# Optimization experiments

Hardware: AMD Instinct MI355X
Metric: run time of the kernel (lower is better)

Reference implementation:

```python
import jax, jax.numpy as jnp
import numpy as np

T, B, D = 1024, 64, 1024  # time steps, batch, num_inputs == num_hiddens
SIGMA = 0.01


def setup_inputs() -> dict:
    key = jax.random.key(0)
    ks = jax.random.split(key, 7)
    w = lambda k: (jax.random.normal(k, (D, D), dtype=jnp.float32) * SIGMA)
    return {
        "inputs": jax.random.normal(ks[0], (T, B, D), dtype=jnp.float32),
        "W_xz": w(ks[1]), "W_hz": w(ks[2]), "b_z": jnp.zeros((D,), jnp.float32),
        "W_xr": w(ks[3]), "W_hr": w(ks[4]), "b_r": jnp.zeros((D,), jnp.float32),
        "W_xh": w(ks[5]), "W_hh": w(ks[6]), "b_h": jnp.zeros((D,), jnp.float32),
    }


def reference(inputs, W_xz, W_hz, b_z, W_xr, W_hr, b_r, W_xh, W_hh, b_h):
    # Precompute all input-to-hidden projections in batched GEMMs (T*B rows).
    Xz = jnp.einsum('tbi,ih->tbh', inputs, W_xz) + b_z
    Xr = jnp.einsum('tbi,ih->tbh', inputs, W_xr) + b_r
    Xh = jnp.einsum('tbi,ih->tbh', inputs, W_xh) + b_h

    def step(H, xs):
        xz, xr, xh = xs
        Z = jax.nn.sigmoid(xz + H @ W_hz)
        R = jax.nn.sigmoid(xr + H @ W_hr)
        # torch precedence: R * H @ W_hh == R * (H @ W_hh)
        H_tilde = jnp.tanh(xh + R * (H @ W_hh))
        H_new = Z * H + (1.0 - Z) * H_tilde
        return H_new, H_new

    H0 = jnp.zeros((inputs.shape[1], inputs.shape[2]), dtype=inputs.dtype)
    H_last, outputs = jax.lax.scan(step, H0, (Xz, Xr, Xh))
    return outputs, H_last
```

## Files before the change

kernel.cpp:

```cpp
#include <hip/hip_runtime.h>
#include <hip/hip_bf16.h>
#include <stdint.h>

typedef unsigned int u32;
typedef unsigned short u16;
typedef short bf16x8 __attribute__((ext_vector_type(8)));
typedef float f32x4 __attribute__((ext_vector_type(4)));
typedef u32 u32x4 __attribute__((ext_vector_type(4)));

#define T_STEPS 1024
#define BATCH   64
#define DIM     1024
#define NGRP    8
#define GWG     32
#define NTHR    512

#define CTL_XCNT(x)   ((x)*16)
#define CTL_ARR       128
#define CTL_MODE      144
#define CTL_FLAG(g,w) (256 + ((g)*GWG + (w))*16)
#define CTL_U32       4608

__device__ __forceinline__ u16 f2bf(float f) {
  u32 u = __float_as_uint(f);
  return (u16)((u + 0x7FFFu + ((u >> 16) & 1u)) >> 16);
}
__device__ __forceinline__ float sigm(float x) { return 1.0f / (1.0f + __expf(-x)); }
__device__ __forceinline__ float tanh_f(float x) {
  x = fminf(8.0f, fmaxf(-8.0f, x));
  float e = __expf(2.0f * x);
  return (e - 1.0f) / (e + 1.0f);
}

__global__ void gru_init(u32* ctrl) {
  for (int i = threadIdx.x; i < CTL_U32; i += 512) ctrl[i] = 0;
}

__global__ void gru_xconv(const float* __restrict__ in, u32* __restrict__ xb) {
  size_t i = (size_t)(blockIdx.x * 256 + threadIdx.x) * 8;
  f32x4 lo = *(const f32x4*)(in + i);
  f32x4 hi = *(const f32x4*)(in + i + 4);
  u32x4 o;
  o[0] = ((u32)f2bf(lo[1]) << 16) | f2bf(lo[0]);
  o[1] = ((u32)f2bf(lo[3]) << 16) | f2bf(lo[2]);
  o[2] = ((u32)f2bf(hi[1]) << 16) | f2bf(hi[0]);
  o[3] = ((u32)f2bf(hi[3]) << 16) | f2bf(hi[2]);
  *(u32x4*)(xb + i / 2) = o;
}

__global__ void gru_pack3(const float* __restrict__ Wz, const float* __restrict__ Wr,
                          const float* __restrict__ Wh, u16* __restrict__ wp) {
  int idx = blockIdx.x * 256 + threadIdx.x;
  if (idx >= GWG * 8 * 2 * 3 * 4 * 64) return;
  int lane = idx & 63; int r = idx >> 6;
  int ks = r & 3; r >>= 2;
  int n = r % 3; r /= 3;
  int cg = r & 1; r >>= 1;
  int wv = r & 7; int wid = r >> 3;
  int k0 = wv * 128 + ks * 32 + (lane >> 4) * 8;
  int col = wid * 32 + cg * 16 + (lane & 15);
  const float* W = (n == 0) ? Wz : (n == 1) ? Wr : Wh;
  u16* dst = wp + (size_t)idx * 8;
#pragma unroll
  for (int j = 0; j < 8; ++j) dst[j] = f2bf(W[(size_t)(k0 + j) * DIM + col]);
}

#define WAIT0 asm volatile("s_waitcnt vmcnt(0)" ::: "memory"); __builtin_amdgcn_sched_barrier(0)
#define MFMA_(A, B, C) __builtin_amdgcn_mfma_f32_16x16x32_bf16(__builtin_bit_cast(bf16x8, A), B, C, 0, 0, 0)

template <int MODE>
__device__ __forceinline__ void scan_run(
    int g, int wid, const u32* __restrict__ xbf,
    const float* __restrict__ bz, const float* __restrict__ br, const float* __restrict__ bh,
    const u16* __restrict__ wpackH, const u16* __restrict__ wpackX,
    u32* hbuf, u32* ctrl, float* __restrict__ out,
    float (&part)[8][2][4][64][6]) {
  const int tid = threadIdx.x;
  const int wv = tid >> 6;
  const int lane = tid & 63;
  u32* hgrp = hbuf + (size_t)g * 8192;

  bf16x8 bregH[2][3][4], bregX[2][3][4];
  {
    const u16* wph = wpackH + (size_t)(wid * 8 + wv) * (2 * 3 * 4 * 512);
    const u16* wpx = wpackX + (size_t)(wid * 8 + wv) * (2 * 3 * 4 * 512);
#pragma unroll
    for (int cg = 0; cg < 2; ++cg)
#pragma unroll
      for (int n = 0; n < 3; ++n)
#pragma unroll
        for (int ks = 0; ks < 4; ++ks) {
          const int off = (((cg * 3 + n) * 4 + ks) * 512) + lane * 8;
          bregH[cg][n][ks] = *(const bf16x8*)(wph + off);
          asm volatile("" : "+v"(bregH[cg][n][ks]));
          bregX[cg][n][ks] = *(const bf16x8*)(wpx + off);
          asm volatile("" : "+v"(bregX[cg][n][ks]));
        }
  }

  const int grow = tid >> 4;
  const int cp = tid & 15;
  const int cgg = cp >> 3;
  const int c16 = 2 * (cp & 7);
  const int col0 = wid * 32 + cgg * 16 + c16;
  const float b_z0 = bz[col0], b_z1 = bz[col0 + 1];
  const float b_r0 = br[col0], b_r1 = br[col0 + 1];
  const float b_h0 = bh[col0], b_h1 = bh[col0 + 1];
  const int cell0 = (grow >> 2) * 16 + c16;
  const int wrd = grow & 3;
  float hp0 = 0.f, hp1 = 0.f;

  f32x4 xc[2][3];
#define COMPX(ts) { \
  u32x4 xa0, xa1, xa2, xa3; \
  const u32* xb_ = xbf + (size_t)(ts) * (BATCH * DIM / 2) \
                 + (size_t)(8 * g + (lane & 7)) * (DIM / 2) + wv * 64 + (lane >> 4) * 4; \
  xa0 = *(const u32x4*)(xb_ + 0);  xa1 = *(const u32x4*)(xb_ + 16); \
  xa2 = *(const u32x4*)(xb_ + 32); xa3 = *(const u32x4*)(xb_ + 48); \
  if ((lane & 15) >= 8) { xa0 = (u32x4){0,0,0,0}; xa1 = (u32x4){0,0,0,0}; \
                          xa2 = (u32x4){0,0,0,0}; xa3 = (u32x4){0,0,0,0}; } \
  _Pragma("unroll") for (int cg_ = 0; cg_ < 2; ++cg_) \
  _Pragma("unroll") for (int n_ = 0; n_ < 3; ++n_) { \
    f32x4 a_ = (f32x4){0.f, 0.f, 0.f, 0.f}; \
    a_ = MFMA_(xa0, bregX[cg_][n_][0], a_); \
    a_ = MFMA_(xa1, bregX[cg_][n_][1], a_); \
    a_ = MFMA_(xa2, bregX[cg_][n_][2], a_); \
    a_ = MFMA_(xa3, bregX[cg_][n_][3], a_); \
    xc[cg_][n_] = a_; } }

  COMPX(0);

#pragma unroll 1
  for (int t = 0; t < T_STEPS; ++t) {
    f32x4 vz[2], vr[2], vhh[2];
#pragma unroll
    for (int cg = 0; cg < 2; ++cg) {
      vz[cg] = xc[cg][0]; vr[cg] = xc[cg][1]; vhh[cg] = (f32x4){0.f, 0.f, 0.f, 0.f};
    }

    if (t > 0) {
      const u32* fp = ctrl + CTL_FLAG(g, wv * 4 + (lane & 3));
      for (;;) {
        u32 f;
        asm volatile("global_load_dword %0, %1, off sc0 sc1\n\ts_waitcnt vmcnt(0)"
                     : "=v"(f) : "v"(fp));
        if (__all((lane < 4) ? (int)(f >= (u32)t) : 1)) break;
        __builtin_amdgcn_s_sleep(1);
      }
      asm volatile("" ::: "memory");
      u32x4 ha0, ha1, ha2, ha3;
      const u32* hb = hgrp + (size_t)((t - 1) & 1) * 4096
                    + (size_t)(lane & 7) * 512 + wv * 64 + (lane >> 4) * 4;
      if (MODE == 1) {
        asm volatile("global_load_dwordx4 %0, %1, off sc0" : "=v"(ha0) : "v"(hb));
        asm volatile("global_load_dwordx4 %0, %1, off offset:64 sc0" : "=v"(ha1) : "v"(hb));
        asm volatile("global_load_dwordx4 %0, %1, off offset:128 sc0" : "=v"(ha2) : "v"(hb));
        asm volatile("global_load_dwordx4 %0, %1, off offset:192 sc0" : "=v"(ha3) : "v"(hb));
      } else {
        asm volatile("global_load_dwordx4 %0, %1, off sc0 sc1" : "=v"(ha0) : "v"(hb));
        asm volatile("global_load_dwordx4 %0, %1, off offset:64 sc0 sc1" : "=v"(ha1) : "v"(hb));
        asm volatile("global_load_dwordx4 %0, %1, off offset:128 sc0 sc1" : "=v"(ha2) : "v"(hb));
        asm volatile("global_load_dwordx4 %0, %1, off offset:192 sc0 sc1" : "=v"(ha3) : "v"(hb));
      }
      WAIT0;
      if ((lane & 15) >= 8) { ha0 = (u32x4){0,0,0,0}; ha1 = (u32x4){0,0,0,0};
                              ha2 = (u32x4){0,0,0,0}; ha3 = (u32x4){0,0,0,0}; }
#pragma unroll
      for (int cg = 0; cg < 2; ++cg) {
        vz[cg] = MFMA_(ha0, bregH[cg][0][0], vz[cg]);
        vz[cg] = MFMA_(ha1, bregH[cg][0][1], vz[cg]);
        vz[cg] = MFMA_(ha2, bregH[cg][0][2], vz[cg]);
        vz[cg] = MFMA_(ha3, bregH[cg][0][3], vz[cg]);
        vr[cg] = MFMA_(ha0, bregH[cg][1][0], vr[cg]);
        vr[cg] = MFMA_(ha1, bregH[cg][1][1], vr[cg]);
        vr[cg] = MFMA_(ha2, bregH[cg][1][2], vr[cg]);
        vr[cg] = MFMA_(ha3, bregH[cg][1][3], vr[cg]);
        vhh[cg] = MFMA_(ha0, bregH[cg][2][0], vhh[cg]);
        vhh[cg] = MFMA_(ha1, bregH[cg][2][1], vhh[cg]);
        vhh[cg] = MFMA_(ha2, bregH[cg][2][2], vhh[cg]);
        vhh[cg] = MFMA_(ha3, bregH[cg][2][3], vhh[cg]);
      }
    }

#pragma unroll
    for (int cg = 0; cg < 2; ++cg) {
      *(float2*)&part[wv][cg][0][lane][0] = make_float2(vz[cg][0], vz[cg][1]);
      *(float2*)&part[wv][cg][0][lane][2] = make_float2(vz[cg][2], vz[cg][3]);
      *(float2*)&part[wv][cg][1][lane][0] = make_float2(vr[cg][0], vr[cg][1]);
      *(float2*)&part[wv][cg][1][lane][2] = make_float2(vr[cg][2], vr[cg][3]);
      *(float2*)&part[wv][cg][2][lane][0] = make_float2(xc[cg][2][0], xc[cg][2][1]);
      *(float2*)&part[wv][cg][2][lane][2] = make_float2(xc[cg][2][2], xc[cg][2][3]);
      *(float2*)&part[wv][cg][3][lane][0] = make_float2(vhh[cg][0], vhh[cg][1]);
      *(float2*)&part[wv][cg][3][lane][2] = make_float2(vhh[cg][2], vhh[cg][3]);
    }
    __syncthreads();

    float hn0 = 0.f, hn1 = 0.f;
    if (tid < 128) {
      float sz0 = 0, sz1 = 0, sr0 = 0, sr1 = 0, sx0 = 0, sx1 = 0, sh0 = 0, sh1 = 0;
#pragma unroll
      for (int w = 0; w < 8; ++w) {
        sz0 += part[w][cgg][0][cell0][wrd];     sz1 += part[w][cgg][0][cell0 + 1][wrd];
        sr0 += part[w][cgg][1][cell0][wrd];     sr1 += part[w][cgg][1][cell0 + 1][wrd];
        sx0 += part[w][cgg][2][cell0][wrd];     sx1 += part[w][cgg][2][cell0 + 1][wrd];
        sh0 += part[w][cgg][3][cell0][wrd];     sh1 += part[w][cgg][3][cell0 + 1][wrd];
      }
      float z0 = sigm(sz0 + b_z0), z1 = sigm(sz1 + b_z1);
      float r0 = sigm(sr0 + b_r0), r1 = sigm(sr1 + b_r1);
      float th0 = tanh_f(sx0 + b_h0 + r0 * sh0);
      float th1 = tanh_f(sx1 + b_h1 + r1 * sh1);
      hn0 = z0 * hp0 + (1.f - z0) * th0;
      hn1 = z1 * hp1 + (1.f - z1) * th1;
      hp0 = hn0; hp1 = hn1;
      u32 pk = ((u32)f2bf(hn1) << 16) | f2bf(hn0);
      u32* hpw = hgrp + (size_t)(t & 1) * 4096 + (size_t)grow * 512 + wid * 16 + cp;
      if (MODE == 1)
        asm volatile("global_store_dword %0, %1, off sc0" :: "v"(hpw), "v"(pk) : "memory");
      else
        asm volatile("global_store_dword %0, %1, off sc0 sc1" :: "v"(hpw), "v"(pk) : "memory");
    }
    WAIT0;
    __syncthreads();
    if (tid == 0) {
      u32* fw = ctrl + CTL_FLAG(g, wid);
      u32 tv = (u32)(t + 1);
      asm volatile("global_store_dword %0, %1, off sc0 sc1" :: "v"(fw), "v"(tv) : "memory");
    }
    if (tid < 128) {
      float* op = out + (size_t)t * (BATCH * DIM) + (size_t)(8 * g + grow) * DIM + col0;
      *(float2*)op = make_float2(hn0, hn1);
      if (t == T_STEPS - 1) {
        float* fo = out + (size_t)T_STEPS * (BATCH * DIM) + (size_t)(8 * g + grow) * DIM + col0;
        *(float2*)fo = make_float2(hn0, hn1);
      }
    }
    if (t + 1 < T_STEPS) COMPX(t + 1);
  }
#undef COMPX
}

__launch_bounds__(NTHR, 2)
__global__ void gru_scan(const u32* __restrict__ xbf,
                         const float* __restrict__ bz, const float* __restrict__ br,
                         const float* __restrict__ bh,
                         const u16* __restrict__ wpackH, const u16* __restrict__ wpackX,
                         u32* hbuf, u32* ctrl, float* __restrict__ out) {
  __shared__ float part[8][2][4][64][6];
  __shared__ u32 meta[4];

  if (threadIdx.x == 0) {
    u32 x;
    asm volatile("s_getreg_b32 %0, hwreg(HW_REG_XCC_ID)" : "=s"(x));
    x &= 7;
    u32 tk = __hip_atomic_fetch_add(ctrl + CTL_XCNT(x), 1u,
                                    __ATOMIC_RELAXED, __HIP_MEMORY_SCOPE_AGENT);
    __hip_atomic_fetch_add(ctrl + CTL_ARR, 1u, __ATOMIC_RELEASE, __HIP_MEMORY_SCOPE_AGENT);
    while (__hip_atomic_load(ctrl + CTL_ARR, __ATOMIC_ACQUIRE, __HIP_MEMORY_SCOPE_AGENT)
           < (u32)(NGRP * GWG))
      __builtin_amdgcn_s_sleep(4);
    if (blockIdx.x == 0) {
      u32 uni = 1;
      for (int i = 0; i < 8; ++i)
        if (__hip_atomic_load(ctrl + CTL_XCNT(i), __ATOMIC_RELAXED,
                              __HIP_MEMORY_SCOPE_AGENT) != GWG) uni = 0;
      __hip_atomic_store(ctrl + CTL_MODE, uni ? 1u : 2u,
                         __ATOMIC_RELEASE, __HIP_MEMORY_SCOPE_AGENT);
    }
    u32 m;
    for (;;) {
      m = __hip_atomic_load(ctrl + CTL_MODE, __ATOMIC_ACQUIRE, __HIP_MEMORY_SCOPE_AGENT);
      if (m != 0) break;
      __builtin_amdgcn_s_sleep(4);
    }
    meta[0] = m;
    meta[1] = (m == 1) ? x : (blockIdx.x >> 5);
    meta[2] = (m == 1) ? tk : (blockIdx.x & 31);
  }
  __syncthreads();
  const u32 m = meta[0];
  const int g = (int)meta[1];
  const int wid = (int)meta[2];
  if (m == 1 && wid >= GWG) return;

  if (m == 1) scan_run<1>(g, wid, xbf, bz, br, bh, wpackH, wpackX, hbuf, ctrl, out, part);
  else        scan_run<2>(g, wid, xbf, bz, br, bh, wpackH, wpackX, hbuf, ctrl, out, part);
}

extern "C" void kernel_launch(void* const* d_in, const int* in_sizes, int n_in,
                              void* d_out, int out_size, void* d_ws, size_t ws_size,
                              hipStream_t stream) {
  const float* inputs = (const float*)d_in[0];
  const float* Wxz = (const float*)d_in[1];
  const float* Whz = (const float*)d_in[2];
  const float* bz  = (const float*)d_in[3];
  const float* Wxr = (const float*)d_in[4];
  const float* Whr = (const float*)d_in[5];
  const float* br  = (const float*)d_in[6];
  const float* Wxh = (const float*)d_in[7];
  const float* Whh = (const float*)d_in[8];
  const float* bh  = (const float*)d_in[9];
  float* out = (float*)d_out;

  char* ws = (char*)d_ws;
  u32* ctrl   = (u32*)ws;
  u32* hbuf   = (u32*)(ws + 32768);
  u16* wpackH = (u16*)(ws + 294912);
  u16* wpackX = (u16*)(ws + 294912 + 6291456);
  u32* xbf    = (u32*)(ws + 294912 + 2 * 6291456);
  size_t need = 294912 + 2 * 6291456 + (size_t)T_STEPS * BATCH * DIM * 2;
  if (ws_size < need) return;

  const int pk = GWG * 8 * 2 * 3 * 4 * 64;
  hipLaunchKernelGGL(gru_init, dim3(1), dim3(512), 0, stream, ctrl);
  hipLaunchKernelGGL(gru_pack3, dim3((pk + 255) / 256), dim3(256), 0, stream,
                     Whz, Whr, Whh, wpackH);
  hipLaunchKernelGGL(gru_pack3, dim3((pk + 255) / 256), dim3(256), 0, stream,
                     Wxz, Wxr, Wxh, wpackX);
  hipLaunchKernelGGL(gru_xconv, dim3(T_STEPS * BATCH * DIM / 8 / 256), dim3(256), 0, stream,
                     inputs, xbf);
  hipLaunchKernelGGL(gru_scan, dim3(NGRP * GWG), dim3(NTHR), 0, stream,
                     xbf, bz, br, bh, wpackH, wpackX, hbuf, ctrl, out);
}
```

Before: 6.667 ms.

## Replace step flags with sentinel-filled hidden-state history and fuse input conversion

Cross-workgroup synchronisation moves from per-workgroup flag counters to polling the hidden-state data directly. A full per-timestep history buffer is pre-filled with an all-ones sentinel, and readers spin until no sentinel remains, so the separate flag store, its wait and the double-buffering go away. The fp32-to-bf16 conversion of the inputs is fused into the scan kernel's loads, which drops the separate conversion pass, and the XCC-aware mode selection is removed. The cost is a 128MB memset each call, twice the bytes for x loads, and correctness that relies on no real bf16 pair equalling the sentinel and on store visibility ordering.

```diff
diff --git a/kernel.cpp b/kernel.cpp
--- a/kernel.cpp
+++ b/kernel.cpp
@@ -14,12 +14,7 @@
 #define NGRP    8
 #define GWG     32
 #define NTHR    512
-
-#define CTL_XCNT(x)   ((x)*16)
-#define CTL_ARR       128
-#define CTL_MODE      144
-#define CTL_FLAG(g,w) (256 + ((g)*GWG + (w))*16)
-#define CTL_U32       4608
+#define SENT    0xFFFFFFFFu
 
 __device__ __forceinline__ u16 f2bf(float f) {
   u32 u = __float_as_uint(f);
@@ -30,22 +25,6 @@
   x = fminf(8.0f, fmaxf(-8.0f, x));
   float e = __expf(2.0f * x);
   return (e - 1.0f) / (e + 1.0f);
-}
-
-__global__ void gru_init(u32* ctrl) {
-  for (int i = threadIdx.x; i < CTL_U32; i += 512) ctrl[i] = 0;
-}
-
-__global__ void gru_xconv(const float* __restrict__ in, u32* __restrict__ xb) {
-  size_t i = (size_t)(blockIdx.x * 256 + threadIdx.x) * 8;
-  f32x4 lo = *(const f32x4*)(in + i);
-  f32x4 hi = *(const f32x4*)(in + i + 4);
-  u32x4 o;
-  o[0] = ((u32)f2bf(lo[1]) << 16) | f2bf(lo[0]);
-  o[1] = ((u32)f2bf(lo[3]) << 16) | f2bf(lo[2]);
-  o[2] = ((u32)f2bf(hi[1]) << 16) | f2bf(hi[0]);
-  o[3] = ((u32)f2bf(hi[3]) << 16) | f2bf(hi[2]);
-  *(u32x4*)(xb + i / 2) = o;
 }
 
 __global__ void gru_pack3(const float* __restrict__ Wz, const float* __restrict__ Wr,
@@ -67,18 +46,21 @@
 
 #define WAIT0 asm volatile("s_waitcnt vmcnt(0)" ::: "memory"); __builtin_amdgcn_sched_barrier(0)
 #define MFMA_(A, B, C) __builtin_amdgcn_mfma_f32_16x16x32_bf16(__builtin_bit_cast(bf16x8, A), B, C, 0, 0, 0)
-
-template <int MODE>
-__device__ __forceinline__ void scan_run(
-    int g, int wid, const u32* __restrict__ xbf,
-    const float* __restrict__ bz, const float* __restrict__ br, const float* __restrict__ bh,
-    const u16* __restrict__ wpackH, const u16* __restrict__ wpackX,
-    u32* hbuf, u32* ctrl, float* __restrict__ out,
-    float (&part)[8][2][4][64][6]) {
+#define PK2(a, b) ((((u32)f2bf(b)) << 16) | (u32)f2bf(a))
+
+__launch_bounds__(NTHR, 2)
+__global__ void gru_scan(const float* __restrict__ inputs,
+                         const float* __restrict__ bz, const float* __restrict__ br,
+                         const float* __restrict__ bh,
+                         const u16* __restrict__ wpackH, const u16* __restrict__ wpackX,
+                         u32* hhist, float* __restrict__ out) {
+  __shared__ float part[8][2][4][64][6];
+
   const int tid = threadIdx.x;
+  const int g   = blockIdx.x >> 5;
+  const int wid = blockIdx.x & 31;
   const int wv = tid >> 6;
   const int lane = tid & 63;
-  u32* hgrp = hbuf + (size_t)g * 8192;
 
   bf16x8 bregH[2][3][4], bregX[2][3][4];
   {
@@ -113,10 +95,17 @@
   f32x4 xc[2][3];
 #define COMPX(ts) { \
   u32x4 xa0, xa1, xa2, xa3; \
-  const u32* xb_ = xbf + (size_t)(ts) * (BATCH * DIM / 2) \
-                 + (size_t)(8 * g + (lane & 7)) * (DIM / 2) + wv * 64 + (lane >> 4) * 4; \
-  xa0 = *(const u32x4*)(xb_ + 0);  xa1 = *(const u32x4*)(xb_ + 16); \
-  xa2 = *(const u32x4*)(xb_ + 32); xa3 = *(const u32x4*)(xb_ + 48); \
+  const float* xb_ = inputs + (size_t)(ts) * (BATCH * DIM) \
+                   + (size_t)(8 * g + (lane & 7)) * DIM + wv * 128 + (lane >> 4) * 8; \
+  { f32x4 lo, hi; \
+    lo = *(const f32x4*)(xb_ + 0);  hi = *(const f32x4*)(xb_ + 4); \
+    xa0[0]=PK2(lo[0],lo[1]); xa0[1]=PK2(lo[2],lo[3]); xa0[2]=PK2(hi[0],hi[1]); xa0[3]=PK2(hi[2],hi[3]); \
+    lo = *(const f32x4*)(xb_ + 32); hi = *(const f32x4*)(xb_ + 36); \
+    xa1[0]=PK2(lo[0],lo[1]); xa1[1]=PK2(lo[2],lo[3]); xa1[2]=PK2(hi[0],hi[1]); xa1[3]=PK2(hi[2],hi[3]); \
+    lo = *(const f32x4*)(xb_ + 64); hi = *(const f32x4*)(xb_ + 68); \
+    xa2[0]=PK2(lo[0],lo[1]); xa2[1]=PK2(lo[2],lo[3]); xa2[2]=PK2(hi[0],hi[1]); xa2[3]=PK2(hi[2],hi[3]); \
+    lo = *(const f32x4*)(xb_ + 96); hi = *(const f32x4*)(xb_ + 100); \
+    xa3[0]=PK2(lo[0],lo[1]); xa3[1]=PK2(lo[2],lo[3]); xa3[2]=PK2(hi[0],hi[1]); xa3[3]=PK2(hi[2],hi[3]); } \
   if ((lane & 15) >= 8) { xa0 = (u32x4){0,0,0,0}; xa1 = (u32x4){0,0,0,0}; \
                           xa2 = (u32x4){0,0,0,0}; xa3 = (u32x4){0,0,0,0}; } \
   _Pragma("unroll") for (int cg_ = 0; cg_ < 2; ++cg_) \
@@ -139,30 +128,27 @@
     }
 
     if (t > 0) {
-      const u32* fp = ctrl + CTL_FLAG(g, wv * 4 + (lane & 3));
+      const u32* hb = hhist + ((size_t)(t - 1) * NGRP + g) * 4096
+                    + (size_t)(lane & 7) * 512 + wv * 64 + (lane >> 4) * 4;
+      u32x4 ha0, ha1, ha2, ha3;
       for (;;) {
-        u32 f;
-        asm volatile("global_load_dword %0, %1, off sc0 sc1\n\ts_waitcnt vmcnt(0)"
-                     : "=v"(f) : "v"(fp));
-        if (__all((lane < 4) ? (int)(f >= (u32)t) : 1)) break;
-        __builtin_amdgcn_s_sleep(1);
-      }
-      asm volatile("" ::: "memory");
-      u32x4 ha0, ha1, ha2, ha3;
-      const u32* hb = hgrp + (size_t)((t - 1) & 1) * 4096
-                    + (size_t)(lane & 7) * 512 + wv * 64 + (lane >> 4) * 4;
-      if (MODE == 1) {
-        asm volatile("global_load_dwordx4 %0, %1, off sc0" : "=v"(ha0) : "v"(hb));
-        asm volatile("global_load_dwordx4 %0, %1, off offset:64 sc0" : "=v"(ha1) : "v"(hb));
-        asm volatile("global_load_dwordx4 %0, %1, off offset:128 sc0" : "=v"(ha2) : "v"(hb));
-        asm volatile("global_load_dwordx4 %0, %1, off offset:192 sc0" : "=v"(ha3) : "v"(hb));
-      } else {
         asm volatile("global_load_dwordx4 %0, %1, off sc0 sc1" : "=v"(ha0) : "v"(hb));
         asm volatile("global_load_dwordx4 %0, %1, off offset:64 sc0 sc1" : "=v"(ha1) : "v"(hb));
         asm volatile("global_load_dwordx4 %0, %1, off offset:128 sc0 sc1" : "=v"(ha2) : "v"(hb));
         asm volatile("global_load_dwordx4 %0, %1, off offset:192 sc0 sc1" : "=v"(ha3) : "v"(hb));
-      }
-      WAIT0;
+        WAIT0;
+        u32 bad = (u32)(ha0[0] == SENT) | (u32)(ha0[1] == SENT)
+                | (u32)(ha0[2] == SENT) | (u32)(ha0[3] == SENT)
+                | (u32)(ha1[0] == SENT) | (u32)(ha1[1] == SENT)
+                | (u32)(ha1[2] == SENT) | (u32)(ha1[3] == SENT)
+                | (u32)(ha2[0] == SENT) | (u32)(ha2[1] == SENT)
+                | (u32)(ha2[2] == SENT) | (u32)(ha2[3] == SENT)
+                | (u32)(ha3[0] == SENT) | (u32)(ha3[1] == SENT)
+                | (u32)(ha3[2] == SENT) | (u32)(ha3[3] == SENT);
+        if (__all((int)(bad == 0))) break;
+        __builtin_amdgcn_s_sleep(1);
+      }
+      asm volatile("" ::: "memory");
       if ((lane & 15) >= 8) { ha0 = (u32x4){0,0,0,0}; ha1 = (u32x4){0,0,0,0};
                               ha2 = (u32x4){0,0,0,0}; ha3 = (u32x4){0,0,0,0}; }
 #pragma unroll
@@ -213,19 +199,11 @@
       hn1 = z1 * hp1 + (1.f - z1) * th1;
       hp0 = hn0; hp1 = hn1;
       u32 pk = ((u32)f2bf(hn1) << 16) | f2bf(hn0);
-      u32* hpw = hgrp + (size_t)(t & 1) * 4096 + (size_t)grow * 512 + wid * 16 + cp;
-      if (MODE == 1)
-        asm volatile("global_store_dword %0, %1, off sc0" :: "v"(hpw), "v"(pk) : "memory");
-      else
-        asm volatile("global_store_dword %0, %1, off sc0 sc1" :: "v"(hpw), "v"(pk) : "memory");
-    }
-    WAIT0;
+      u32* hpw = hhist + ((size_t)t * NGRP + g) * 4096 + (size_t)grow * 512 + wid * 16 + cp;
+      asm volatile("global_store_dword %0, %1, off sc0 sc1" :: "v"(hpw), "v"(pk) : "memory");
+    }
     __syncthreads();
-    if (tid == 0) {
-      u32* fw = ctrl + CTL_FLAG(g, wid);
-      u32 tv = (u32)(t + 1);
-      asm volatile("global_store_dword %0, %1, off sc0 sc1" :: "v"(fw), "v"(tv) : "memory");
-    }
+
     if (tid < 128) {
       float* op = out + (size_t)t * (BATCH * DIM) + (size_t)(8 * g + grow) * DIM + col0;
       *(float2*)op = make_float2(hn0, hn1);
@@ -237,53 +215,6 @@
     if (t + 1 < T_STEPS) COMPX(t + 1);
   }
 #undef COMPX
-}
-
-__launch_bounds__(NTHR, 2)
-__global__ void gru_scan(const u32* __restrict__ xbf,
-                         const float* __restrict__ bz, const float* __restrict__ br,
-                         const float* __restrict__ bh,
-                         const u16* __restrict__ wpackH, const u16* __restrict__ wpackX,
-                         u32* hbuf, u32* ctrl, float* __restrict__ out) {
-  __shared__ float part[8][2][4][64][6];
-  __shared__ u32 meta[4];
-
-  if (threadIdx.x == 0) {
-    u32 x;
-    asm volatile("s_getreg_b32 %0, hwreg(HW_REG_XCC_ID)" : "=s"(x));
-    x &= 7;
-    u32 tk = __hip_atomic_fetch_add(ctrl + CTL_XCNT(x), 1u,
-                                    __ATOMIC_RELAXED, __HIP_MEMORY_SCOPE_AGENT);
-    __hip_atomic_fetch_add(ctrl + CTL_ARR, 1u, __ATOMIC_RELEASE, __HIP_MEMORY_SCOPE_AGENT);
-    while (__hip_atomic_load(ctrl + CTL_ARR, __ATOMIC_ACQUIRE, __HIP_MEMORY_SCOPE_AGENT)
-           < (u32)(NGRP * GWG))
-      __builtin_amdgcn_s_sleep(4);
-    if (blockIdx.x == 0) {
-      u32 uni = 1;
-      for (int i = 0; i < 8; ++i)
-        if (__hip_atomic_load(ctrl + CTL_XCNT(i), __ATOMIC_RELAXED,
-                              __HIP_MEMORY_SCOPE_AGENT) != GWG) uni = 0;
-      __hip_atomic_store(ctrl + CTL_MODE, uni ? 1u : 2u,
-                         __ATOMIC_RELEASE, __HIP_MEMORY_SCOPE_AGENT);
-    }
-    u32 m;
-    for (;;) {
-      m = __hip_atomic_load(ctrl + CTL_MODE, __ATOMIC_ACQUIRE, __HIP_MEMORY_SCOPE_AGENT);
-      if (m != 0) break;
-      __builtin_amdgcn_s_sleep(4);
-    }
-    meta[0] = m;
-    meta[1] = (m == 1) ? x : (blockIdx.x >> 5);
-    meta[2] = (m == 1) ? tk : (blockIdx.x & 31);
-  }
-  __syncthreads();
-  const u32 m = meta[0];
-  const int g = (int)meta[1];
-  const int wid = (int)meta[2];
-  if (m == 1 && wid >= GWG) return;
-
-  if (m == 1) scan_run<1>(g, wid, xbf, bz, br, bh, wpackH, wpackX, hbuf, ctrl, out, part);
-  else        scan_run<2>(g, wid, xbf, bz, br, bh, wpackH, wpackX, hbuf, ctrl, out, part);
 }
 
 extern "C" void kernel_launch(void* const* d_in, const int* in_sizes, int n_in,
@@ -302,22 +233,20 @@
   float* out = (float*)d_out;
 
   char* ws = (char*)d_ws;
-  u32* ctrl   = (u32*)ws;
-  u32* hbuf   = (u32*)(ws + 32768);
-  u16* wpackH = (u16*)(ws + 294912);
-  u16* wpackX = (u16*)(ws + 294912 + 6291456);
-  u32* xbf    = (u32*)(ws + 294912 + 2 * 6291456);
-  size_t need = 294912 + 2 * 6291456 + (size_t)T_STEPS * BATCH * DIM * 2;
+  u32* hhist  = (u32*)ws;
+  size_t hhist_bytes = (size_t)T_STEPS * NGRP * 4096 * 4;
+  u16* wpackH = (u16*)(ws + hhist_bytes);
+  u16* wpackX = (u16*)(ws + hhist_bytes + 6291456);
+  size_t need = hhist_bytes + 2 * 6291456;
   if (ws_size < need) return;
 
+  hipMemsetAsync(hhist, 0xFF, hhist_bytes, stream);
+
   const int pk = GWG * 8 * 2 * 3 * 4 * 64;
-  hipLaunchKernelGGL(gru_init, dim3(1), dim3(512), 0, stream, ctrl);
   hipLaunchKernelGGL(gru_pack3, dim3((pk + 255) / 256), dim3(256), 0, stream,
                      Whz, Whr, Whh, wpackH);
   hipLaunchKernelGGL(gru_pack3, dim3((pk + 255) / 256), dim3(256), 0, stream,
                      Wxz, Wxr, Wxh, wpackX);
-  hipLaunchKernelGGL(gru_xconv, dim3(T_STEPS * BATCH * DIM / 8 / 256), dim3(256), 0, stream,
-                     inputs, xbf);
   hipLaunchKernelGGL(gru_scan, dim3(NGRP * GWG), dim3(NTHR), 0, stream,
-                     xbf, bz, br, bh, wpackH, wpackX, hbuf, ctrl, out);
-}
+                     inputs, bz, br, bh, wpackH, wpackX, hhist, out);
+}
```

Result: slower. 7.553 ms (+13.3%).
